# Optimization experiments

Hardware: AMD Instinct MI355X
Metric: run time of the kernel (lower is better)

## Reference

```python
import jax, jax.numpy as jnp
import numpy as np

N = 100000      # nodes
E = 1600000     # edges (before self-loops)
F_IN = 128      # dataset.num_features
H1 = 128        # hidden_channels/2
H2 = 256        # hidden_channels
C = 40          # dataset.num_classes
EPS = 1e-5      # BatchNorm eps
NEG_SLOPE = 0.2 # GATConv leaky_relu slope


def setup_inputs() -> dict:
    key = jax.random.key(0)
    ks = jax.random.split(key, 12)
    p = lambda k, shape: jax.random.normal(k, shape, jnp.float32) * 0.1
    x = jax.random.normal(ks[0], (N, F_IN), jnp.float32)
    edge_index = jax.random.randint(ks[1], (2, E), 0, N, dtype=jnp.int64)
    return dict(
        x=x, edge_index=edge_index,
        w1=p(ks[2], (F_IN, H1)), as1=p(ks[3], (H1,)), ad1=p(ks[4], (H1,)), b1=jnp.zeros(H1, jnp.float32),
        g1=jnp.ones(H1, jnp.float32), be1=jnp.zeros(H1, jnp.float32), rm1=jnp.zeros(H1, jnp.float32), rv1=jnp.ones(H1, jnp.float32),
        w2=p(ks[5], (H1, H2)), as2=p(ks[6], (H2,)), ad2=p(ks[7], (H2,)), b2=jnp.zeros(H2, jnp.float32),
        g2=jnp.ones(H2, jnp.float32), be2=jnp.zeros(H2, jnp.float32), rm2=jnp.zeros(H2, jnp.float32), rv2=jnp.ones(H2, jnp.float32),
        w3=p(ks[8], (H2, C)), as3=p(ks[9], (C,)), ad3=p(ks[10], (C,)), b3=jnp.zeros(C, jnp.float32),
    )


def gat_conv(x, src, dst, W, a_src, a_dst, b):
    """PyG GATConv (heads=1, add_self_loops already applied to src/dst)."""
    h = x @ W                                  # [N, F_out]
    alpha_src = h @ a_src                      # [N]
    alpha_dst = h @ a_dst                      # [N]
    logits = jax.nn.leaky_relu(alpha_src[src] + alpha_dst[dst], NEG_SLOPE)  # [E']
    # segment softmax over incoming edges of each dst node
    m = jax.ops.segment_max(logits, dst, num_segments=N)
    e = jnp.exp(logits - m[dst])
    denom = jax.ops.segment_sum(e, dst, num_segments=N)
    alpha = e / denom[dst]                     # [E']
    out = jax.ops.segment_sum(h[src] * alpha[:, None], dst, num_segments=N)
    return out + b


def bn_eval(x, gamma, beta, mean, var):
    return (x - mean) * jax.lax.rsqrt(var + EPS) * gamma + beta


def reference(x, edge_index,
              w1, as1, ad1, b1, g1, be1, rm1, rv1,
              w2, as2, ad2, b2, g2, be2, rm2, rv2,
              w3, as3, ad3, b3):
    # add self-loops once (PyG GATConv default add_self_loops=True)
    loop = jnp.arange(N, dtype=edge_index.dtype)
    src = jnp.concatenate([edge_index[0], loop])
    dst = jnp.concatenate([edge_index[1], loop])
    # eval mode: dropout is identity, BN uses running stats
    h = gat_conv(x, src, dst, w1, as1, ad1, b1)
    h = jnp.tanh(bn_eval(h, g1, be1, rm1, rv1))
    h = gat_conv(h, src, dst, w2, as2, ad2, b2)
    h = jnp.tanh(bn_eval(h, g2, be2, rm2, rv2))
    return gat_conv(h, src, dst, w3, as3, ad3, b3)
```

## Files before the change

### kernel.cpp

```cpp
#include <hip/hip_runtime.h>
#include <hip/hip_bf16.h>
#include <cstddef>

#define N_NODES 100000
#define E_EDGES 1600000
#define TOT_EDGES (E_EDGES + N_NODES)
#define NEG_SLOPE 0.2f
#define BN_EPS 1e-5f
#define NBKT ((N_NODES + 255) / 256)
#define NBA 512

typedef __attribute__((ext_vector_type(8))) short short8;
typedef __attribute__((ext_vector_type(4))) float f32x4;
typedef __attribute__((ext_vector_type(2))) float f32x2;
typedef __attribute__((ext_vector_type(4))) int int32x4;
typedef __attribute__((ext_vector_type(2))) int int32x2;

#if defined(__has_builtin)
#if __has_builtin(__builtin_amdgcn_make_buffer_rsrc) && __has_builtin(__builtin_amdgcn_raw_buffer_load_b128)
#define HAVE_BUFRSRC 1
#endif
#if __has_builtin(__builtin_amdgcn_make_buffer_rsrc) && __has_builtin(__builtin_amdgcn_raw_buffer_load_b64)
#define HAVE_BUF64 1
#endif
#endif

__device__ __forceinline__ unsigned short f2bf(float f) {
    union { float f; unsigned u; } c; c.f = f;
    unsigned u = c.u;
    u += 0x7fffu + ((u >> 16) & 1u);
    return (unsigned short)(u >> 16);
}
__device__ __forceinline__ float bf2f(unsigned short h) {
    union { unsigned u; float f; } c; c.u = ((unsigned)h) << 16;
    return c.f;
}
__device__ __forceinline__ unsigned short f2h(float f) {
    union { _Float16 h; unsigned short u; } c; c.h = (_Float16)f; return c.u;
}
__device__ __forceinline__ float lrelu(float t) {
    return (t > 0.f) ? t : NEG_SLOPE * t;
}
__device__ __forceinline__ float tanh_fast(float x) {
    float e = __expf(2.f * x);
    return 1.f - 2.f / (e + 1.f);
}
__device__ __forceinline__ unsigned short pk_fp8(float a, float b) {
    unsigned v;
    asm volatile("v_cvt_pk_fp8_f32 %0, %1, %2" : "=v"(v) : "v"(a), "v"(b));
    return (unsigned short)v;
}
__device__ __forceinline__ f32x2 unpk_fp8(unsigned u) {
    f32x2 r;
    asm volatile("v_cvt_pk_f32_fp8 %0, %1" : "=v"(r) : "v"(u));
    return r;
}

__device__ __forceinline__ float wave_sum63(float x) {
    x += __int_as_float(__builtin_amdgcn_update_dpp(0, __float_as_int(x), 0x111, 0xf, 0xf, true));
    x += __int_as_float(__builtin_amdgcn_update_dpp(0, __float_as_int(x), 0x112, 0xf, 0xf, true));
    x += __int_as_float(__builtin_amdgcn_update_dpp(0, __float_as_int(x), 0x114, 0xf, 0xf, true));
    x += __int_as_float(__builtin_amdgcn_update_dpp(0, __float_as_int(x), 0x118, 0xf, 0xf, true));
    x += __int_as_float(__builtin_amdgcn_update_dpp(0, __float_as_int(x), 0x142, 0xf, 0xf, true));
    x += __int_as_float(__builtin_amdgcn_update_dpp(0, __float_as_int(x), 0x143, 0xf, 0xf, true));
    return x;
}
__device__ __forceinline__ float wave_sum_bcast(float x) {
    return __int_as_float(__builtin_amdgcn_readlane(__float_as_int(wave_sum63(x)), 63));
}


__global__ __launch_bounds__(256) void csr_hist(const int* __restrict__ ei,
                                                int* __restrict__ bh) {
    __shared__ int h[NBKT];
    int t = threadIdx.x;
    for (int b = t; b < NBKT; b += 256) h[b] = 0;
    __syncthreads();
    int idx = blockIdx.x * 256 + t;
    const int stride = NBA * 256;
    for (int e = idx; e < TOT_EDGES; e += stride) {
        int d = (e < E_EDGES) ? ei[E_EDGES + e] : (e - E_EDGES);
        atomicAdd(&h[((unsigned)d) >> 8], 1);
    }
    __syncthreads();
    for (int b = t; b < NBKT; b += 256) bh[blockIdx.x * NBKT + b] = h[b];
}

__global__ __launch_bounds__(512) void csr_scan_blocks(int* __restrict__ bh,
                                                       int* __restrict__ totals) {
    __shared__ int s[NBA];
    int t = threadIdx.x, bin = blockIdx.x;
    int v = bh[t * NBKT + bin];
    s[t] = v;
    __syncthreads();
    for (int off = 1; off < NBA; off <<= 1) {
        int y = (t >= off) ? s[t - off] : 0;
        __syncthreads();
        s[t] += y;
        __syncthreads();
    }
    bh[t * NBKT + bin] = s[t] - v;
    if (t == NBA - 1) totals[bin] = s[t];
}

__global__ __launch_bounds__(512) void csr_scan_buckets(const int* __restrict__ totals,
                                                        int* __restrict__ starts) {
    __shared__ int s[512];
    int t = threadIdx.x;
    int v = (t < NBKT) ? totals[t] : 0;
    s[t] = v;
    __syncthreads();
    for (int off = 1; off < 512; off <<= 1) {
        int y = (t >= off) ? s[t - off] : 0;
        __syncthreads();
        s[t] += y;
        __syncthreads();
    }
    if (t < NBKT) starts[t] = s[t] - v;
    if (t == 0) starts[NBKT] = TOT_EDGES;
}

__global__ __launch_bounds__(256) void csr_scatter(const int* __restrict__ ei,
                                                   const int* __restrict__ bh,
                                                   const int* __restrict__ starts,
                                                   int* __restrict__ pairs) {
    __shared__ int wp[NBKT];
    int t = threadIdx.x;
    for (int b = t; b < NBKT; b += 256)
        wp[b] = starts[b] + bh[blockIdx.x * NBKT + b];
    __syncthreads();
    int idx = blockIdx.x * 256 + t;
    const int stride = NBA * 256;
    for (int e = idx; e < TOT_EDGES; e += stride) {
        int s, d;
        if (e < E_EDGES) { s = ei[e]; d = ei[E_EDGES + e]; }
        else             { s = e - E_EDGES; d = s; }
        int pos = atomicAdd(&wp[((unsigned)d) >> 8], 1);
        pairs[pos] = s | ((d & 255) << 20);
    }
}

__global__ __launch_bounds__(256) void csr_build(const int* __restrict__ pairs,
                                                 const int* __restrict__ starts,
                                                 int* __restrict__ row_ptr,
                                                 int* __restrict__ src_sorted) {
    __shared__ int nh[256];
    __shared__ int sc[256];
    __shared__ int wp[256];
    int k = blockIdx.x, t = threadIdx.x;
    int bs = starts[k], be = starts[k + 1];
    nh[t] = 0;
    __syncthreads();
    for (int i = bs + t; i < be; i += 256)
        atomicAdd(&nh[((unsigned)pairs[i]) >> 20], 1);
    __syncthreads();
    int v = nh[t];
    sc[t] = v;
    __syncthreads();
    for (int off = 1; off < 256; off <<= 1) {
        int y = (t >= off) ? sc[t - off] : 0;
        __syncthreads();
        sc[t] += y;
        __syncthreads();
    }
    int excl = sc[t] - v;
    int node = k * 256 + t;
    if (node <= N_NODES) row_ptr[node] = bs + excl;
    wp[t] = bs + excl;
    __syncthreads();
    for (int i = bs + t; i < be; i += 256) {
        unsigned p = (unsigned)pairs[i];
        int pos = atomicAdd(&wp[p >> 20], 1);
        src_sorted[pos] = (int)(p & 0xFFFFFu);
    }
}


__global__ __launch_bounds__(256) void xconv_frag(const float* __restrict__ x,
                                                  unsigned short* __restrict__ hi,
                                                  unsigned short* __restrict__ lo) {
    const size_t CSTRIDE = (size_t)N_NODES * 32;
    int idx = blockIdx.x * blockDim.x + threadIdx.x;
    int stride = gridDim.x * blockDim.x;
    const int n = N_NODES * 128;
    for (int i = idx; i < n; i += stride) {
        float v = x[i];
        int row = i >> 7, f = i & 127;
        size_t a = (size_t)(f >> 5) * CSTRIDE + (size_t)row * 32 + (f & 31);
        unsigned short h = f2bf(v);
        hi[a] = h;
        lo[a] = f2bf(v - bf2f(h));
    }
}

__global__ __launch_bounds__(256) void wprep_all(
    const float* __restrict__ w1, const float* __restrict__ w2, const float* __restrict__ w3,
    const float* __restrict__ as1, const float* __restrict__ ad1,
    const float* __restrict__ as2, const float* __restrict__ ad2,
    const float* __restrict__ as3, const float* __restrict__ ad3,
    unsigned short* __restrict__ w1th, unsigned short* __restrict__ w1tl,
    unsigned short* __restrict__ w2th, unsigned short* __restrict__ w2tl,
    unsigned short* __restrict__ w3th, unsigned short* __restrict__ w3tl,
    unsigned short* __restrict__ ab1h, unsigned short* __restrict__ ab1l,
    unsigned short* __restrict__ ab3h, unsigned short* __restrict__ ab3l,
    float* __restrict__ ws2f, float* __restrict__ wd2f) {
    const int T1 = 128 * 128, T2 = 256 * 128, T3 = 48 * 256;
    const int W = T1 + T2 + T3;
    int idx = blockIdx.x * 256 + threadIdx.x;
    if (idx < W) {
        float v; unsigned short* th; unsigned short* tl; int o;
        if (idx < T1) {
            int n = idx / 128, k = idx % 128;
            v = w1[k * 128 + n]; th = w1th; tl = w1tl; o = idx;
        } else if (idx < T1 + T2) {
            int i = idx - T1; int n = i / 128, k = i % 128;
            v = w2[k * 256 + n]; th = w2th; tl = w2tl; o = i;
        } else {
            int i = idx - T1 - T2; int n = i / 256, k = i % 256;
            v = (n < 40) ? w3[k * 40 + n] : 0.f; th = w3th; tl = w3tl; o = i;
        }
        unsigned short h = f2bf(v);
        th[o] = h;
        tl[o] = f2bf(v - bf2f(h));
        return;
    }
    int j = idx - W;
    if (j < 2048) {
        int r = j / 128, k = j % 128;
        float v = 0.f;
        if (r < 2) {
            const float* a = r ? ad1 : as1;
            const float* wr = w1 + (size_t)k * 128;
            for (int n = 0; n < 128; n++) v += wr[n] * a[n];
        }
        unsigned short h = f2bf(v);
        ab1h[j] = h; ab1l[j] = f2bf(v - bf2f(h));
    } else if (j < 2048 + 4096) {
        int i = j - 2048; int r = i / 256, k = i % 256;
        float v = 0.f;
        if (r < 2) {
            const float* a = r ? ad3 : as3;
            const float* wr = w3 + (size_t)k * 40;
            for (int n = 0; n < 40; n++) v += wr[n] * a[n];
        }
        unsigned short h = f2bf(v);
        ab3h[i] = h; ab3l[i] = f2bf(v - bf2f(h));
    } else if (j < 2048 + 4096 + 256) {
        int i = j - 2048 - 4096; int r = i / 128, k = i % 128;
        const float* a = r ? ad2 : as2;
        const float* wr = w2 + (size_t)k * 256;
        float v = 0.f;
        for (int n = 0; n < 256; n++) v += wr[n] * a[n];
        if (r == 0) ws2f[k] = v; else wd2f[k] = v;
    }
}

template<int K, int NTILES, int MWAVES, int NWAVES, int NACT, bool ASPLIT, bool ALPHA, bool BNT, bool CFRAG, bool CHALF>
__global__ __launch_bounds__(256) void mfma_gemm(
    const unsigned short* __restrict__ Ahi, const unsigned short* __restrict__ Alo,
    const unsigned short* __restrict__ BThi, const unsigned short* __restrict__ BTlo,
    const unsigned short* __restrict__ ABh, const unsigned short* __restrict__ ABl,
    unsigned short* __restrict__ Chi, int ldc,
    const float* __restrict__ bias, const float* __restrict__ gamma,
    const float* __restrict__ beta, const float* __restrict__ rmean,
    const float* __restrict__ rvar,
    float* __restrict__ asrc, float* __restrict__ adst, int M)
{
    int lane = threadIdx.x & 63;
    int wave = threadIdx.x >> 6;
    int quad = lane >> 4;
    int l16  = lane & 15;
    long mbase = (long)blockIdx.x * (64 * MWAVES) + (long)(wave / NWAVES) * 64;
    int n0 = ((wave % NWAVES) + blockIdx.y * NWAVES) * (NTILES * 16);
    bool aw = ((wave % NWAVES) == 0) && (blockIdx.y == 0);
    const size_t CSTRIDE = (size_t)M * 32;

    size_t roff[4];
#pragma unroll
    for (int i = 0; i < 4; i++) {
        long r = mbase + i * 16 + l16;
        if (r > M - 1) r = M - 1;
        roff[i] = (size_t)r * 32 + (size_t)(quad * 8);
    }
    const unsigned short* bh[NTILES]; const unsigned short* bl[NTILES];
#pragma unroll
    for (int j = 0; j < NTILES; j++) {
        long n = n0 + j * 16 + l16;
        bh[j] = BThi + n * K; bl[j] = BTlo + n * K;
    }
    const unsigned short* bah = nullptr; const unsigned short* bal = nullptr;
    if constexpr (ALPHA) { bah = ABh + (size_t)l16 * K; bal = ABl + (size_t)l16 * K; }
    const int ko = quad * 8;

    f32x4 acc[4][NTILES];
    f32x4 acca[4];
#pragma unroll
    for (int i = 0; i < 4; i++) {
        acca[i] = (f32x4){0.f, 0.f, 0.f, 0.f};
#pragma unroll
        for (int j = 0; j < NTILES; j++)
            acc[i][j] = (f32x4){0.f, 0.f, 0.f, 0.f};
    }

    for (int kc = 0; kc < K / 32; kc++) {
        const int k0 = kc * 32;
        const unsigned short* Ah = Ahi + (size_t)kc * CSTRIDE;
        const unsigned short* Al = ASPLIT ? (Alo + (size_t)kc * CSTRIDE) : nullptr;
        short8 vah[4], vall[4], vbh[NTILES], vbl[NTILES];
#pragma unroll
        for (int i = 0; i < 4; i++) {
            vah[i] = *(const short8*)(Ah + roff[i]);
            if constexpr (ASPLIT) vall[i] = *(const short8*)(Al + roff[i]);
        }
#pragma unroll
        for (int j = 0; j < NTILES; j++) {
            vbh[j] = *(const short8*)(bh[j] + k0 + ko);
            vbl[j] = *(const short8*)(bl[j] + k0 + ko);
        }
#pragma unroll
        for (int i = 0; i < 4; i++)
#pragma unroll
            for (int j = 0; j < NTILES; j++) {
                acc[i][j] = __builtin_amdgcn_mfma_f32_16x16x32_bf16(vah[i], vbh[j], acc[i][j], 0, 0, 0);
                acc[i][j] = __builtin_amdgcn_mfma_f32_16x16x32_bf16(vah[i], vbl[j], acc[i][j], 0, 0, 0);
                if constexpr (ASPLIT)
                    acc[i][j] = __builtin_amdgcn_mfma_f32_16x16x32_bf16(vall[i], vbh[j], acc[i][j], 0, 0, 0);
            }
        if constexpr (ALPHA) {
            if (aw) {
                short8 vbah = *(const short8*)(bah + k0 + ko);
                short8 vbal = *(const short8*)(bal + k0 + ko);
#pragma unroll
                for (int i = 0; i < 4; i++) {
                    acca[i] = __builtin_amdgcn_mfma_f32_16x16x32_bf16(vah[i], vbah, acca[i], 0, 0, 0);
                    acca[i] = __builtin_amdgcn_mfma_f32_16x16x32_bf16(vah[i], vbal, acca[i], 0, 0, 0);
                    if constexpr (ASPLIT)
                        acca[i] = __builtin_amdgcn_mfma_f32_16x16x32_bf16(vall[i], vbah, acca[i], 0, 0, 0);
                }
            }
        }
    }

#pragma unroll
    for (int i = 0; i < 4; i++)
#pragma unroll
        for (int j = 0; j < NTILES; j++) {
            int col = n0 + j * 16 + l16;
            float bb = 0.f, rs = 1.f, gg = 1.f, bt = 0.f, rm = 0.f;
            if constexpr (BNT) {
                bb = bias[col]; gg = gamma[col]; bt = beta[col];
                rm = rmean[col]; rs = rsqrtf(rvar[col] + BN_EPS);
            }
#pragma unroll
            for (int r = 0; r < 4; r++) {
                long row = mbase + i * 16 + quad * 4 + r;
                if (row < M && col < NACT) {
                    float v = acc[i][j][r];
                    if constexpr (BNT) v = tanh_fast((v + bb - rm) * rs * gg + bt);
                    if constexpr (CFRAG) {
                        Chi[(size_t)(col >> 5) * CSTRIDE + (size_t)row * 32 + (col & 31)] = f2bf(v);
                    } else {
                        Chi[row * ldc + col] = CHALF ? f2h(v) : f2bf(v);
                    }
                }
            }
        }
    if constexpr (ALPHA) {
        if (aw) {
#pragma unroll
            for (int i = 0; i < 4; i++)
#pragma unroll
                for (int r = 0; r < 4; r++) {
                    long row = mbase + i * 16 + quad * 4 + r;
                    if (row < M) {
                        float v = acca[i][r];
                        if (l16 == 0) asrc[row] = v;
                        else if (l16 == 1) adst[row] = v;
                    }
                }
        }
    }
}

template<int MODE>
__global__ __launch_bounds__(256) void gat_agg_wide(
    const unsigned short* __restrict__ hsrc,
    const float* __restrict__ asrc, const float* __restrict__ adst,
    const int* __restrict__ row_ptr, const int* __restrict__ src_sorted,
    const float* __restrict__ bias, const float* __restrict__ gamma,
    const float* __restrict__ beta, const float* __restrict__ rmean,
    const float* __restrict__ rvar,
    const float* __restrict__ wsn, const float* __restrict__ wdn,
    unsigned short* __restrict__ ohi,
    float* __restrict__ outf,
    float* __restrict__ asrc_n, float* __restrict__ adst_n)
{
    constexpr int SH  = (MODE == 0) ? 8 : 7;
    constexpr int BPL = (MODE == 0) ? 16 : 8;
    constexpr int NF  = (MODE == 2) ? 4 : 8;

    __shared__ __align__(16) float2 esw[4][64];
    __shared__ __align__(16) float red[4][4][132];

    int wave = threadIdx.x >> 6;
    int lane = threadIdx.x & 63;
    int node = blockIdx.x * 4 + wave;
    if (node >= N_NODES) return;

    int start = row_ptr[node];
    int end = row_ptr[node + 1];
    int deg = end - start;
    float ad = adst[node];
    int sub = lane >> 4;
    int foff = (lane & 15) * BPL;
    int tpos = (lane & 3) * 16 + (lane >> 2);

#if defined(HAVE_BUFRSRC) && defined(HAVE_BUF64)
    auto rsrc = __builtin_amdgcn_make_buffer_rsrc((void*)hsrc, (short)0,
                                                  N_NODES << SH, 0x00020000);
#endif

    float acc[NF];
#pragma unroll
    for (int i = 0; i < NF; i++) acc[i] = 0.f;

    auto ld = [&](int vo) {
        if constexpr (MODE == 0) {
#if defined(HAVE_BUFRSRC) && defined(HAVE_BUF64)
            return __builtin_amdgcn_raw_buffer_load_b128(rsrc, vo, 0, 0);
#else
            return *reinterpret_cast<const int32x4*>(
                reinterpret_cast<const char*>(hsrc) + (unsigned)vo);
#endif
        } else {
#if defined(HAVE_BUFRSRC) && defined(HAVE_BUF64)
            return __builtin_amdgcn_raw_buffer_load_b64(rsrc, vo, 0, 0);
#else
            return *reinterpret_cast<const int32x2*>(
                reinterpret_cast<const char*>(hsrc) + (unsigned)vo);
#endif
        }
    };
    auto fmaN = [&](auto u, float ww) {
        if constexpr (MODE == 0) {
            union { decltype(u) v; unsigned w[4]; } c; c.v = u;
#pragma unroll
            for (int i = 0; i < 4; i++) {
                union { unsigned u; _Float16 h[2]; } t; t.u = c.w[i];
                acc[2 * i]     += ww * (float)t.h[0];
                acc[2 * i + 1] += ww * (float)t.h[1];
            }
        } else if constexpr (MODE == 1) {
            union { decltype(u) v; unsigned w[2]; } c; c.v = u;
#pragma unroll
            for (int i = 0; i < 2; i++) {
                f32x2 lo = unpk_fp8(c.w[i]);
                f32x2 hi = unpk_fp8(c.w[i] >> 16);
                acc[4 * i]     += ww * lo.x;
                acc[4 * i + 1] += ww * lo.y;
                acc[4 * i + 2] += ww * hi.x;
                acc[4 * i + 3] += ww * hi.y;
            }
        } else {
            union { decltype(u) v; unsigned w[2]; } c; c.v = u;
#pragma unroll
            for (int i = 0; i < 2; i++) {
                union { unsigned u; _Float16 h[2]; } t; t.u = c.w[i];
                acc[2 * i]     += ww * (float)t.h[0];
                acc[2 * i + 1] += ww * (float)t.h[1];
            }
        }
    };
    auto gather = [&](int nst) {
        const float2* ep = &esw[wave][sub * 16];
#pragma unroll
        for (int b = 0; b < 4; b++) {
            int s0 = b * 4;
            if (s0 < nst) {
                f32x4 p01 = *(const f32x4*)(ep + s0);
                f32x4 p23 = *(const f32x4*)(ep + s0 + 2);
                bool g1 = s0 + 1 < nst, g2 = s0 + 2 < nst, g3 = s0 + 3 < nst;
                auto u0 = ld(__float_as_int(p01.x) + foff);
                decltype(u0) u1, u2, u3;
                if (g1) u1 = ld(__float_as_int(p01.z) + foff);
                if (g2) u2 = ld(__float_as_int(p23.x) + foff);
                if (g3) u3 = ld(__float_as_int(p23.z) + foff);
                fmaN(u0, p01.y);
                if (g1) fmaN(u1, p01.w);
                if (g2) fmaN(u2, p23.y);
                if (g3) fmaN(u3, p23.w);
            }
        }
    };

    if (deg <= 64) {
        int e = start + lane;
        int s = 0; float w = 0.f;
        if (e < end) { s = src_sorted[e]; w = __expf(lrelu(asrc[s] + ad)); }
        float dsum = wave_sum_bcast(w);
        esw[wave][tpos] = make_float2(__int_as_float(s << SH), w * (1.0f / dsum));
        gather((deg + 3) >> 2);
    } else {
        float part = 0.f;
        for (int cs = start; cs < end; cs += 64) {
            int e = cs + lane;
            if (e < end) part += __expf(lrelu(asrc[src_sorted[e]] + ad));
        }
        float inv = 1.0f / wave_sum_bcast(part);
        for (int cs = start; cs < end; cs += 64) {
            int e = cs + lane;
            int s = 0; float w = 0.f;
            if (e < end) { s = src_sorted[e]; w = __expf(lrelu(asrc[s] + ad)) * inv; }
            esw[wave][tpos] = make_float2(__int_as_float(s << SH), w);
            gather((min(64, end - cs) + 3) >> 2);
        }
    }

    if constexpr (MODE == 2) {
        *reinterpret_cast<f32x4*>(&red[wave][sub][(lane & 15) * 4]) =
            (f32x4){acc[0], acc[1], acc[2], acc[3]};
        float t = 0.f;
#pragma unroll
        for (int g = 0; g < 4; g++) t += red[wave][g][lane];
        if (lane < 40) outf[(size_t)node * 40 + lane] = t + bias[lane];
    } else {
        f32x4* dst = reinterpret_cast<f32x4*>(&red[wave][sub][(lane & 15) * 8]);
        dst[0] = (f32x4){acc[0], acc[1], acc[2], acc[3]};
        dst[1] = (f32x4){acc[4], acc[5], acc[6], acc[7]};
        f32x2 tsum = (f32x2){0.f, 0.f};
#pragma unroll
        for (int g = 0; g < 4; g++)
            tsum += *reinterpret_cast<const f32x2*>(&red[wave][g][lane * 2]);

        if constexpr (MODE == 0) {
            float vals[2];
#pragma unroll
            for (int v = 0; v < 2; v++) {
                int f = lane * 2 + v;
                float val = tsum[v] + bias[f];
                float rs = rsqrtf(rvar[f] + BN_EPS);
                vals[v] = tanh_fast((val - rmean[f]) * rs * gamma[f] + beta[f]);
            }
            ohi[(size_t)node * 64 + lane] = pk_fp8(vals[0], vals[1]);
            float ps = vals[0] * wsn[lane * 2] + vals[1] * wsn[lane * 2 + 1];
            float pd = vals[0] * wdn[lane * 2] + vals[1] * wdn[lane * 2 + 1];
            ps = wave_sum63(ps);
            pd = wave_sum63(pd);
            if (lane == 63) { asrc_n[node] = ps; adst_n[node] = pd; }
        } else {
            const size_t CSTRIDE = (size_t)N_NODES * 32;
            unsigned w0 = (unsigned)f2bf(tsum[0]) | ((unsigned)f2bf(tsum[1]) << 16);
            size_t a = (size_t)(lane >> 4) * CSTRIDE + (size_t)node * 32 + ((lane * 2) & 31);
            *reinterpret_cast<unsigned*>(ohi + a) = w0;
        }
    }
}


static inline size_t align256(size_t x) { return (x + 255) & ~(size_t)255; }

extern "C" void kernel_launch(void* const* d_in, const int* in_sizes, int n_in,
                              void* d_out, int out_size, void* d_ws, size_t ws_size,
                              hipStream_t stream) {
    const float* x   = (const float*)d_in[0];
    const int* ei    = (const int*)d_in[1];
    const float* w1  = (const float*)d_in[2];
    const float* as1 = (const float*)d_in[3];
    const float* ad1 = (const float*)d_in[4];
    const float* b1  = (const float*)d_in[5];
    const float* g1  = (const float*)d_in[6];
    const float* be1 = (const float*)d_in[7];
    const float* rm1 = (const float*)d_in[8];
    const float* rv1 = (const float*)d_in[9];
    const float* w2  = (const float*)d_in[10];
    const float* as2 = (const float*)d_in[11];
    const float* ad2 = (const float*)d_in[12];
    const float* b2  = (const float*)d_in[13];
    const float* g2  = (const float*)d_in[14];
    const float* be2 = (const float*)d_in[15];
    const float* rm2 = (const float*)d_in[16];
    const float* rv2 = (const float*)d_in[17];
    const float* w3  = (const float*)d_in[18];
    const float* as3 = (const float*)d_in[19];
    const float* ad3 = (const float*)d_in[20];
    const float* b3  = (const float*)d_in[21];
    float* out = (float*)d_out;

    const size_t P128 = align256((size_t)N_NODES * 128 * 2);
    const size_t P256 = align256((size_t)N_NODES * 256 * 2);

    char* p = (char*)d_ws;
    char* regA = p; p += P256;
    char* regB = p; p += P256;
    unsigned short* xhi  = (unsigned short*)regA;
    unsigned short* xlo  = (unsigned short*)(regA + P128);
    unsigned short* o1p  = (unsigned short*)regA;
    unsigned short* o2hi = (unsigned short*)regA;
    unsigned short* h1h  = (unsigned short*)regB;
    unsigned short* g2hi = (unsigned short*)regB;
    unsigned short* h3h  = (unsigned short*)regB;
    int* pairs  = (int*)regB;
    int* bhist  = (int*)(regB + align256((size_t)TOT_EDGES * 4));
    int* totals = (int*)((char*)bhist + align256((size_t)NBA * NBKT * 4));
    int* starts = (int*)((char*)totals + align256((size_t)NBKT * 4));

    float* asrcA = (float*)p; p += align256((size_t)N_NODES * 4);
    float* adstA = (float*)p; p += align256((size_t)N_NODES * 4);
    float* asrcB = (float*)p; p += align256((size_t)N_NODES * 4);
    float* adstB = (float*)p; p += align256((size_t)N_NODES * 4);
    int* row_ptr   = (int*)p; p += align256((size_t)(N_NODES + 1) * 4);
    int* src_sorted = (int*)p; p += align256((size_t)TOT_EDGES * 4);
    unsigned short* w1th = (unsigned short*)p; p += align256(128 * 128 * 2);
    unsigned short* w1tl = (unsigned short*)p; p += align256(128 * 128 * 2);
    unsigned short* w2th = (unsigned short*)p; p += align256(256 * 128 * 2);
    unsigned short* w2tl = (unsigned short*)p; p += align256(256 * 128 * 2);
    unsigned short* w3th = (unsigned short*)p; p += align256(48 * 256 * 2);
    unsigned short* w3tl = (unsigned short*)p; p += align256(48 * 256 * 2);
    unsigned short* ab1h = (unsigned short*)p; p += align256(16 * 128 * 2);
    unsigned short* ab1l = (unsigned short*)p; p += align256(16 * 128 * 2);
    unsigned short* ab3h = (unsigned short*)p; p += align256(16 * 256 * 2);
    unsigned short* ab3l = (unsigned short*)p; p += align256(16 * 256 * 2);
    float* ws2f = (float*)p; p += align256(128 * 4);
    float* wd2f = (float*)p; p += align256(128 * 4);

    const int WTOT = 128 * 128 + 256 * 128 + 48 * 256 + 2048 + 4096 + 256;

    xconv_frag<<<4096, 256, 0, stream>>>(x, xhi, xlo);
    wprep_all<<<(WTOT + 255) / 256, 256, 0, stream>>>(
        w1, w2, w3, as1, ad1, as2, ad2, as3, ad3,
        w1th, w1tl, w2th, w2tl, w3th, w3tl,
        ab1h, ab1l, ab3h, ab3l, ws2f, wd2f);

    csr_hist<<<NBA, 256, 0, stream>>>(ei, bhist);
    csr_scan_blocks<<<NBKT, 512, 0, stream>>>(bhist, totals);
    csr_scan_buckets<<<1, 512, 0, stream>>>(totals, starts);
    csr_scatter<<<NBA, 256, 0, stream>>>(ei, bhist, starts, pairs);
    csr_build<<<NBKT, 256, 0, stream>>>(pairs, starts, row_ptr, src_sorted);

    const int NWB = (N_NODES + 3) / 4;
    const int G64 = (N_NODES + 63) / 64;
    const int G256 = (N_NODES + 255) / 256;

    mfma_gemm<128, 2, 1, 4, 128, true, true, false, false, true><<<G64, 256, 0, stream>>>(
        xhi, xlo, w1th, w1tl, ab1h, ab1l, h1h, 128,
        nullptr, nullptr, nullptr, nullptr, nullptr, asrcA, adstA, N_NODES);
    gat_agg_wide<0><<<NWB, 256, 0, stream>>>(
        h1h, asrcA, adstA, row_ptr, src_sorted,
        b1, g1, be1, rm1, rv1, ws2f, wd2f,
        o1p, nullptr, asrcB, adstB);

    gat_agg_wide<1><<<NWB, 256, 0, stream>>>(
        o1p, asrcB, adstB, row_ptr, src_sorted,
        nullptr, nullptr, nullptr, nullptr, nullptr, nullptr, nullptr,
        g2hi, nullptr, nullptr, nullptr);
    mfma_gemm<128, 2, 1, 4, 256, false, false, true, true, false><<<dim3(G64, 2), 256, 0, stream>>>(
        g2hi, nullptr, w2th, w2tl, nullptr, nullptr, o2hi, 256,
        b2, g2, be2, rm2, rv2, nullptr, nullptr, N_NODES);

    mfma_gemm<256, 3, 4, 1, 48, false, true, false, false, true><<<G256, 256, 0, stream>>>(
        o2hi, nullptr, w3th, w3tl, ab3h, ab3l, h3h, 64,
        nullptr, nullptr, nullptr, nullptr, nullptr, asrcA, adstA, N_NODES);
    gat_agg_wide<2><<<NWB, 256, 0, stream>>>(
        h3h, asrcA, adstA, row_ptr, src_sorted,
        b3, nullptr, nullptr, nullptr, nullptr, nullptr, nullptr,
        nullptr, out, nullptr, nullptr);
}
```

Baseline: 462.9 us.

## Split GAT aggregation into edge-weight pass and feature-sliced gather kernels

Each fused aggregation kernel is replaced by two kernels. One computes normalized softmax edge weights per edge into a buffer. The second gathers neighbour features per feature slice with 4-byte loads, so each block touches only a narrow column slice, aiming for better cache locality. Layer 3 output is stored in a plane layout of 8-column slices, and layer-1 attention dot products are reduced across slices in an extra kernel. This adds kernel launches, an edge-weight round trip through memory, and redundant row_ptr and edge-weight reads for every slice.

```diff
diff --git a/kernel.cpp b/kernel.cpp
--- a/kernel.cpp
+++ b/kernel.cpp
@@ -17,11 +17,8 @@
 typedef __attribute__((ext_vector_type(2))) int int32x2;
 
 #if defined(__has_builtin)
-#if __has_builtin(__builtin_amdgcn_make_buffer_rsrc) && __has_builtin(__builtin_amdgcn_raw_buffer_load_b128)
-#define HAVE_BUFRSRC 1
-#endif
-#if __has_builtin(__builtin_amdgcn_make_buffer_rsrc) && __has_builtin(__builtin_amdgcn_raw_buffer_load_b64)
-#define HAVE_BUF64 1
+#if __has_builtin(__builtin_amdgcn_make_buffer_rsrc) && __has_builtin(__builtin_amdgcn_raw_buffer_load_b32)
+#define HAVE_BUF32 1
 #endif
 #endif
 
@@ -255,7 +252,7 @@
     }
 }
 
-template<int K, int NTILES, int MWAVES, int NWAVES, int NACT, bool ASPLIT, bool ALPHA, bool BNT, bool CFRAG, bool CHALF>
+template<int K, int NTILES, int MWAVES, int NWAVES, int NACT, bool ASPLIT, bool ALPHA, bool BNT, bool CFRAG, bool CHALF, bool CPLANE>
 __global__ __launch_bounds__(256) void mfma_gemm(
     const unsigned short* __restrict__ Ahi, const unsigned short* __restrict__ Alo,
     const unsigned short* __restrict__ BThi, const unsigned short* __restrict__ BTlo,
@@ -359,6 +356,8 @@
                     if constexpr (BNT) v = tanh_fast((v + bb - rm) * rs * gg + bt);
                     if constexpr (CFRAG) {
                         Chi[(size_t)(col >> 5) * CSTRIDE + (size_t)row * 32 + (col & 31)] = f2bf(v);
+                    } else if constexpr (CPLANE) {
+                        Chi[(size_t)(col >> 3) * ((size_t)M * 8) + (size_t)row * 8 + (col & 7)] = f2h(v);
                     } else {
                         Chi[row * ldc + col] = CHALF ? f2h(v) : f2bf(v);
                     }
@@ -382,178 +381,207 @@
     }
 }
 
-template<int MODE>
-__global__ __launch_bounds__(256) void gat_agg_wide(
-    const unsigned short* __restrict__ hsrc,
+__global__ __launch_bounds__(256) void gat_ew(
     const float* __restrict__ asrc, const float* __restrict__ adst,
     const int* __restrict__ row_ptr, const int* __restrict__ src_sorted,
+    float2* __restrict__ ew)
+{
+    int wave = threadIdx.x >> 6;
+    int lane = threadIdx.x & 63;
+    int node = blockIdx.x * 4 + wave;
+    if (node >= N_NODES) return;
+    int start = row_ptr[node];
+    int end = row_ptr[node + 1];
+    int deg = end - start;
+    float ad = adst[node];
+
+    if (deg <= 64) {
+        int e = start + lane;
+        int s = 0; float w = 0.f;
+        if (e < end) { s = src_sorted[e]; w = __expf(lrelu(asrc[s] + ad)); }
+        float dsum = wave_sum_bcast(w);
+        if (e < end) ew[e] = make_float2(__int_as_float(s), w / dsum);
+    } else {
+        float part = 0.f;
+        for (int cs = start; cs < end; cs += 64) {
+            int e = cs + lane;
+            if (e < end) part += __expf(lrelu(asrc[src_sorted[e]] + ad));
+        }
+        float inv = 1.0f / wave_sum_bcast(part);
+        for (int cs = start; cs < end; cs += 64) {
+            int e = cs + lane;
+            if (e < end) {
+                int s = src_sorted[e];
+                ew[e] = make_float2(__int_as_float(s), __expf(lrelu(asrc[s] + ad)) * inv);
+            }
+        }
+    }
+}
+
+template<int L>
+__global__ __launch_bounds__(256) void gat_agg_slice(
+    const unsigned short* __restrict__ hsrc,
+    const float2* __restrict__ ew,
+    const int* __restrict__ row_ptr,
     const float* __restrict__ bias, const float* __restrict__ gamma,
     const float* __restrict__ beta, const float* __restrict__ rmean,
     const float* __restrict__ rvar,
     const float* __restrict__ wsn, const float* __restrict__ wdn,
     unsigned short* __restrict__ ohi,
     float* __restrict__ outf,
-    float* __restrict__ asrc_n, float* __restrict__ adst_n)
+    float2* __restrict__ pdot)
 {
-    constexpr int SH  = (MODE == 0) ? 8 : 7;
-    constexpr int BPL = (MODE == 0) ? 16 : 8;
-    constexpr int NF  = (MODE == 2) ? 4 : 8;
-
-    __shared__ __align__(16) float2 esw[4][64];
-    __shared__ __align__(16) float red[4][4][132];
-
+    constexpr int SLICES = (L == 3) ? 5 : 8;
+    constexpr int LPELOG = (L == 1) ? 3 : 2;
+    constexpr int LPE = 1 << LPELOG;
+    constexpr int EPS = 64 / LPE;
+    constexpr int FPL = (L == 2) ? 4 : 2;
+    constexpr int SF  = LPE * FPL;
+    constexpr int ROWSH = (L == 1) ? 8 : (L == 2) ? 7 : 4;
+    constexpr int TBYTES = (L == 1) ? N_NODES * 256
+                         : (L == 2) ? N_NODES * 128 : N_NODES * 16 * 5;
+
+    __shared__ float red[4][16][17];
+    __shared__ float vsh[4][16];
+
+    int b = blockIdx.x;
+    int slice = (L == 3) ? (b % 5) : (b & 7);
+    int g     = (L == 3) ? (b / 5) : (b >> 3);
     int wave = threadIdx.x >> 6;
     int lane = threadIdx.x & 63;
-    int node = blockIdx.x * 4 + wave;
-    if (node >= N_NODES) return;
-
-    int start = row_ptr[node];
-    int end = row_ptr[node + 1];
-    int deg = end - start;
-    float ad = adst[node];
-    int sub = lane >> 4;
-    int foff = (lane & 15) * BPL;
-    int tpos = (lane & 3) * 16 + (lane >> 2);
-
-#if defined(HAVE_BUFRSRC) && defined(HAVE_BUF64)
+    int sub  = lane >> LPELOG;
+    int li   = lane & (LPE - 1);
+
+    int sliceoff;
+    if constexpr (L == 1)      sliceoff = slice * 32 + li * 4;
+    else if constexpr (L == 2) sliceoff = slice * 16 + li * 4;
+    else                       sliceoff = slice * (N_NODES * 16) + li * 4;
+
+#ifdef HAVE_BUF32
     auto rsrc = __builtin_amdgcn_make_buffer_rsrc((void*)hsrc, (short)0,
-                                                  N_NODES << SH, 0x00020000);
+                                                  TBYTES, 0x00020000);
 #endif
-
-    float acc[NF];
-#pragma unroll
-    for (int i = 0; i < NF; i++) acc[i] = 0.f;
-
-    auto ld = [&](int vo) {
-        if constexpr (MODE == 0) {
-#if defined(HAVE_BUFRSRC) && defined(HAVE_BUF64)
-            return __builtin_amdgcn_raw_buffer_load_b128(rsrc, vo, 0, 0);
+    auto ld = [&](int vo) -> unsigned {
+#ifdef HAVE_BUF32
+        return __builtin_amdgcn_raw_buffer_load_b32(rsrc, vo, 0, 0);
 #else
-            return *reinterpret_cast<const int32x4*>(
-                reinterpret_cast<const char*>(hsrc) + (unsigned)vo);
+        return *reinterpret_cast<const unsigned*>(
+            reinterpret_cast<const char*>(hsrc) + (unsigned)vo);
 #endif
-        } else {
-#if defined(HAVE_BUFRSRC) && defined(HAVE_BUF64)
-            return __builtin_amdgcn_raw_buffer_load_b64(rsrc, vo, 0, 0);
-#else
-            return *reinterpret_cast<const int32x2*>(
-                reinterpret_cast<const char*>(hsrc) + (unsigned)vo);
-#endif
-        }
     };
-    auto fmaN = [&](auto u, float ww) {
-        if constexpr (MODE == 0) {
-            union { decltype(u) v; unsigned w[4]; } c; c.v = u;
-#pragma unroll
-            for (int i = 0; i < 4; i++) {
-                union { unsigned u; _Float16 h[2]; } t; t.u = c.w[i];
-                acc[2 * i]     += ww * (float)t.h[0];
-                acc[2 * i + 1] += ww * (float)t.h[1];
+
+#pragma unroll
+    for (int p = 0; p < 2; p++) {
+        int node = g * 8 + p * 4 + wave;
+        if (node < N_NODES) {
+            int start = row_ptr[node];
+            int end   = row_ptr[node + 1];
+
+            float acc[FPL];
+#pragma unroll
+            for (int i = 0; i < FPL; i++) acc[i] = 0.f;
+
+            for (int e0 = start; e0 < end; e0 += 4 * EPS) {
+                float2 q[4]; bool act[4]; float wk[4]; unsigned u[4];
+#pragma unroll
+                for (int k = 0; k < 4; k++) {
+                    act[k] = (e0 + k * EPS) < end;
+                    if (act[k]) {
+                        int e = e0 + k * EPS + sub;
+                        int idx = min(e, end - 1);
+                        q[k] = ew[idx];
+                        wk[k] = (e < end) ? q[k].y : 0.f;
+                    }
+                }
+#pragma unroll
+                for (int k = 0; k < 4; k++)
+                    if (act[k])
+                        u[k] = ld((__float_as_int(q[k].x) << ROWSH) + sliceoff);
+#pragma unroll
+                for (int k = 0; k < 4; k++) {
+                    if (act[k]) {
+                        if constexpr (L == 2) {
+                            f32x2 lo = unpk_fp8(u[k]);
+                            f32x2 hi = unpk_fp8(u[k] >> 16);
+                            acc[0] += wk[k] * lo.x;
+                            acc[1] += wk[k] * lo.y;
+                            acc[2] += wk[k] * hi.x;
+                            acc[3] += wk[k] * hi.y;
+                        } else {
+                            union { unsigned u; _Float16 h[2]; } t; t.u = u[k];
+                            acc[0] += wk[k] * (float)t.h[0];
+                            acc[1] += wk[k] * (float)t.h[1];
+                        }
+                    }
+                }
             }
-        } else if constexpr (MODE == 1) {
-            union { decltype(u) v; unsigned w[2]; } c; c.v = u;
-#pragma unroll
-            for (int i = 0; i < 2; i++) {
-                f32x2 lo = unpk_fp8(c.w[i]);
-                f32x2 hi = unpk_fp8(c.w[i] >> 16);
-                acc[4 * i]     += ww * lo.x;
-                acc[4 * i + 1] += ww * lo.y;
-                acc[4 * i + 2] += ww * hi.x;
-                acc[4 * i + 3] += ww * hi.y;
+
+#pragma unroll
+            for (int j = 0; j < FPL; j++)
+                red[wave][sub][li * FPL + j] = acc[j];
+
+            if constexpr (L == 1) {
+                float ps = 0.f, pd = 0.f;
+                if (lane < 16) {
+                    float t = 0.f;
+#pragma unroll
+                    for (int gg = 0; gg < EPS; gg++) t += red[wave][gg][lane];
+                    int F = slice * 16 + lane;
+                    float val = t + bias[F];
+                    float rs = rsqrtf(rvar[F] + BN_EPS);
+                    val = tanh_fast((val - rmean[F]) * rs * gamma[F] + beta[F]);
+                    vsh[wave][lane] = val;
+                    ps = val * wsn[F];
+                    pd = val * wdn[F];
+                }
+                ps = wave_sum63(ps);
+                pd = wave_sum63(pd);
+                if (lane == 63) pdot[(size_t)slice * N_NODES + node] = make_float2(ps, pd);
+                if (lane < 8) {
+                    unsigned short v8 = pk_fp8(vsh[wave][2 * lane], vsh[wave][2 * lane + 1]);
+                    ohi[(size_t)node * 64 + slice * 8 + lane] = v8;
+                }
+            } else if constexpr (L == 2) {
+                if (lane < 16) {
+                    float t = 0.f;
+#pragma unroll
+                    for (int gg = 0; gg < EPS; gg++) t += red[wave][gg][lane];
+                    vsh[wave][lane] = t;
+                }
+                if (lane < 8) {
+                    const size_t CSTRIDE = (size_t)N_NODES * 32;
+                    int col0 = slice * 16 + 2 * lane;
+                    unsigned w0 = (unsigned)f2bf(vsh[wave][2 * lane]) |
+                                  ((unsigned)f2bf(vsh[wave][2 * lane + 1]) << 16);
+                    size_t a = (size_t)(col0 >> 5) * CSTRIDE + (size_t)node * 32 + (col0 & 31);
+                    *reinterpret_cast<unsigned*>(ohi + a) = w0;
+                }
+            } else {
+                if (lane < 8) {
+                    float t = 0.f;
+#pragma unroll
+                    for (int gg = 0; gg < EPS; gg++) t += red[wave][gg][lane];
+                    int F = slice * 8 + lane;
+                    outf[(size_t)node * 40 + F] = t + bias[F];
+                }
             }
-        } else {
-            union { decltype(u) v; unsigned w[2]; } c; c.v = u;
-#pragma unroll
-            for (int i = 0; i < 2; i++) {
-                union { unsigned u; _Float16 h[2]; } t; t.u = c.w[i];
-                acc[2 * i]     += ww * (float)t.h[0];
-                acc[2 * i + 1] += ww * (float)t.h[1];
-            }
-        }
-    };
-    auto gather = [&](int nst) {
-        const float2* ep = &esw[wave][sub * 16];
-#pragma unroll
-        for (int b = 0; b < 4; b++) {
-            int s0 = b * 4;
-            if (s0 < nst) {
-                f32x4 p01 = *(const f32x4*)(ep + s0);
-                f32x4 p23 = *(const f32x4*)(ep + s0 + 2);
-                bool g1 = s0 + 1 < nst, g2 = s0 + 2 < nst, g3 = s0 + 3 < nst;
-                auto u0 = ld(__float_as_int(p01.x) + foff);
-                decltype(u0) u1, u2, u3;
-                if (g1) u1 = ld(__float_as_int(p01.z) + foff);
-                if (g2) u2 = ld(__float_as_int(p23.x) + foff);
-                if (g3) u3 = ld(__float_as_int(p23.z) + foff);
-                fmaN(u0, p01.y);
-                if (g1) fmaN(u1, p01.w);
-                if (g2) fmaN(u2, p23.y);
-                if (g3) fmaN(u3, p23.w);
-            }
-        }
-    };
-
-    if (deg <= 64) {
-        int e = start + lane;
-        int s = 0; float w = 0.f;
-        if (e < end) { s = src_sorted[e]; w = __expf(lrelu(asrc[s] + ad)); }
-        float dsum = wave_sum_bcast(w);
-        esw[wave][tpos] = make_float2(__int_as_float(s << SH), w * (1.0f / dsum));
-        gather((deg + 3) >> 2);
-    } else {
-        float part = 0.f;
-        for (int cs = start; cs < end; cs += 64) {
-            int e = cs + lane;
-            if (e < end) part += __expf(lrelu(asrc[src_sorted[e]] + ad));
-        }
-        float inv = 1.0f / wave_sum_bcast(part);
-        for (int cs = start; cs < end; cs += 64) {
-            int e = cs + lane;
-            int s = 0; float w = 0.f;
-            if (e < end) { s = src_sorted[e]; w = __expf(lrelu(asrc[s] + ad)) * inv; }
-            esw[wave][tpos] = make_float2(__int_as_float(s << SH), w);
-            gather((min(64, end - cs) + 3) >> 2);
-        }
-    }
-
-    if constexpr (MODE == 2) {
-        *reinterpret_cast<f32x4*>(&red[wave][sub][(lane & 15) * 4]) =
-            (f32x4){acc[0], acc[1], acc[2], acc[3]};
-        float t = 0.f;
-#pragma unroll
-        for (int g = 0; g < 4; g++) t += red[wave][g][lane];
-        if (lane < 40) outf[(size_t)node * 40 + lane] = t + bias[lane];
-    } else {
-        f32x4* dst = reinterpret_cast<f32x4*>(&red[wave][sub][(lane & 15) * 8]);
-        dst[0] = (f32x4){acc[0], acc[1], acc[2], acc[3]};
-        dst[1] = (f32x4){acc[4], acc[5], acc[6], acc[7]};
-        f32x2 tsum = (f32x2){0.f, 0.f};
-#pragma unroll
-        for (int g = 0; g < 4; g++)
-            tsum += *reinterpret_cast<const f32x2*>(&red[wave][g][lane * 2]);
-
-        if constexpr (MODE == 0) {
-            float vals[2];
-#pragma unroll
-            for (int v = 0; v < 2; v++) {
-                int f = lane * 2 + v;
-                float val = tsum[v] + bias[f];
-                float rs = rsqrtf(rvar[f] + BN_EPS);
-                vals[v] = tanh_fast((val - rmean[f]) * rs * gamma[f] + beta[f]);
-            }
-            ohi[(size_t)node * 64 + lane] = pk_fp8(vals[0], vals[1]);
-            float ps = vals[0] * wsn[lane * 2] + vals[1] * wsn[lane * 2 + 1];
-            float pd = vals[0] * wdn[lane * 2] + vals[1] * wdn[lane * 2 + 1];
-            ps = wave_sum63(ps);
-            pd = wave_sum63(pd);
-            if (lane == 63) { asrc_n[node] = ps; adst_n[node] = pd; }
-        } else {
-            const size_t CSTRIDE = (size_t)N_NODES * 32;
-            unsigned w0 = (unsigned)f2bf(tsum[0]) | ((unsigned)f2bf(tsum[1]) << 16);
-            size_t a = (size_t)(lane >> 4) * CSTRIDE + (size_t)node * 32 + ((lane * 2) & 31);
-            *reinterpret_cast<unsigned*>(ohi + a) = w0;
-        }
-    }
+        }
+    }
+}
+
+__global__ __launch_bounds__(256) void pdot_reduce(const float2* __restrict__ pdot,
+                                                   float* __restrict__ asrc_n,
+                                                   float* __restrict__ adst_n) {
+    int i = blockIdx.x * 256 + threadIdx.x;
+    if (i >= N_NODES) return;
+    float ps = 0.f, pd = 0.f;
+#pragma unroll
+    for (int s = 0; s < 8; s++) {
+        float2 t = pdot[(size_t)s * N_NODES + i];
+        ps += t.x; pd += t.y;
+    }
+    asrc_n[i] = ps;
+    adst_n[i] = pd;
 }
 
 
@@ -596,9 +624,11 @@
     unsigned short* xlo  = (unsigned short*)(regA + P128);
     unsigned short* o1p  = (unsigned short*)regA;
     unsigned short* o2hi = (unsigned short*)regA;
+    float2* pdot = (float2*)(regA + P128);
     unsigned short* h1h  = (unsigned short*)regB;
     unsigned short* g2hi = (unsigned short*)regB;
     unsigned short* h3h  = (unsigned short*)regB;
+    float2* ewbuf = (float2*)(regB + P128);
     int* pairs  = (int*)regB;
     int* bhist  = (int*)(regB + align256((size_t)TOT_EDGES * 4));
     int* totals = (int*)((char*)bhist + align256((size_t)NBA * NBKT * 4));
@@ -640,28 +670,34 @@
     const int NWB = (N_NODES + 3) / 4;
     const int G64 = (N_NODES + 63) / 64;
     const int G256 = (N_NODES + 255) / 256;
-
-    mfma_gemm<128, 2, 1, 4, 128, true, true, false, false, true><<<G64, 256, 0, stream>>>(
+    const int NG8 = (N_NODES + 7) / 8;
+    const int NBL = (N_NODES + 255) / 256;
+
+    mfma_gemm<128, 2, 1, 4, 128, true, true, false, false, true, false><<<G64, 256, 0, stream>>>(
         xhi, xlo, w1th, w1tl, ab1h, ab1l, h1h, 128,
         nullptr, nullptr, nullptr, nullptr, nullptr, asrcA, adstA, N_NODES);
-    gat_agg_wide<0><<<NWB, 256, 0, stream>>>(
-        h1h, asrcA, adstA, row_ptr, src_sorted,
+    gat_ew<<<NWB, 256, 0, stream>>>(asrcA, adstA, row_ptr, src_sorted, ewbuf);
+    gat_agg_slice<1><<<NG8 * 8, 256, 0, stream>>>(
+        h1h, ewbuf, row_ptr,
         b1, g1, be1, rm1, rv1, ws2f, wd2f,
-        o1p, nullptr, asrcB, adstB);
-
-    gat_agg_wide<1><<<NWB, 256, 0, stream>>>(
-        o1p, asrcB, adstB, row_ptr, src_sorted,
+        o1p, nullptr, pdot);
+    pdot_reduce<<<NBL, 256, 0, stream>>>(pdot, asrcB, adstB);
+
+    gat_ew<<<NWB, 256, 0, stream>>>(asrcB, adstB, row_ptr, src_sorted, ewbuf);
+    gat_agg_slice<2><<<NG8 * 8, 256, 0, stream>>>(
+        o1p, ewbuf, row_ptr,
         nullptr, nullptr, nullptr, nullptr, nullptr, nullptr, nullptr,
-        g2hi, nullptr, nullptr, nullptr);
-    mfma_gemm<128, 2, 1, 4, 256, false, false, true, true, false><<<dim3(G64, 2), 256, 0, stream>>>(
+        g2hi, nullptr, nullptr);
+    mfma_gemm<128, 2, 1, 4, 256, false, false, true, true, false, false><<<dim3(G64, 2), 256, 0, stream>>>(
         g2hi, nullptr, w2th, w2tl, nullptr, nullptr, o2hi, 256,
         b2, g2, be2, rm2, rv2, nullptr, nullptr, N_NODES);
 
-    mfma_gemm<256, 3, 4, 1, 48, false, true, false, false, true><<<G256, 256, 0, stream>>>(
+    mfma_gemm<256, 3, 4, 1, 40, false, true, false, false, true, true><<<G256, 256, 0, stream>>>(
         o2hi, nullptr, w3th, w3tl, ab3h, ab3l, h3h, 64,
         nullptr, nullptr, nullptr, nullptr, nullptr, asrcA, adstA, N_NODES);
-    gat_agg_wide<2><<<NWB, 256, 0, stream>>>(
-        h3h, asrcA, adstA, row_ptr, src_sorted,
+    gat_ew<<<NWB, 256, 0, stream>>>(asrcA, adstA, row_ptr, src_sorted, ewbuf);
+    gat_agg_slice<3><<<NG8 * 5, 256, 0, stream>>>(
+        h3h, ewbuf, row_ptr,
         b3, nullptr, nullptr, nullptr, nullptr, nullptr, nullptr,
-        nullptr, out, nullptr, nullptr);
-}
+        nullptr, out, nullptr);
+}
```

Result: slower. 929.7 us (+100.8%).
